# Kernel tuning notes

Hardware: AMD Instinct MI355X
Metric: run time of the kernel (lower is better)

Reference implementation:

```python
import jax, jax.numpy as jnp
import numpy as np

N = 50000      # nodes per graph type
E = 600000     # directed edges
F = 64         # raw node feature length
H = 128        # hidden / embedding size (embedding == h, so no padding needed)
STEPS = 4
G = 64         # graphs in batch


def setup_inputs() -> dict:
    key = jax.random.key(0)
    ks = jax.random.split(key, 16)
    s = 1.0 / np.sqrt(H)
    inp = {
        "atom_x": jax.random.normal(ks[0], (N, F), jnp.float32),
        "voro_x": jax.random.normal(ks[1], (N, F), jnp.float32),
        "atom_edge_index": jax.random.randint(ks[2], (2, E), 0, N, jnp.int64),
        "voro_edge_index": jax.random.randint(ks[3], (2, E), 0, N, jnp.int64),
        "batch": jnp.sort(jax.random.randint(ks[4], (N,), 0, G, jnp.int64)),
        # input embeddings (bias=False)
        "W_atom_in": jax.random.normal(ks[5], (F, H), jnp.float32) / np.sqrt(F),
        "W_voro_in": jax.random.normal(ks[6], (F, H), jnp.float32) / np.sqrt(F),
        # GatedGraphConv per-step message weights [STEPS, H, H]
        "atom_W": jax.random.normal(ks[7], (STEPS, H, H), jnp.float32) * s,
        "voro_W": jax.random.normal(ks[8], (STEPS, H, H), jnp.float32) * s,
        # GRUCell params (torch layout: W_ih [3H, H], gates ordered r, z, n)
        "atom_Wih": jax.random.normal(ks[9], (3 * H, H), jnp.float32) * s,
        "atom_Whh": jax.random.normal(ks[10], (3 * H, H), jnp.float32) * s,
        "atom_bih": jnp.zeros((3 * H,), jnp.float32),
        "atom_bhh": jnp.zeros((3 * H,), jnp.float32),
        "voro_Wih": jax.random.normal(ks[11], (3 * H, H), jnp.float32) * s,
        "voro_Whh": jax.random.normal(ks[12], (3 * H, H), jnp.float32) * s,
        "voro_bih": jnp.zeros((3 * H,), jnp.float32),
        "voro_bhh": jnp.zeros((3 * H,), jnp.float32),
        # prediction head Linear(2H, 1)
        "pred_W": jax.random.normal(ks[13], (2 * H, 1), jnp.float32) * s,
        "pred_b": jnp.zeros((1,), jnp.float32),
    }
    return inp


def _gated_graph_conv(x, edge_index, W, Wih, Whh, bih, bhh):
    """PyG GatedGraphConv with aggr='add': per step, m = h @ W_l, scatter-add
    messages from source to target, then GRUCell(m, h)."""
    src, dst = edge_index[0], edge_index[1]

    def step(h, Wl):
        m = h @ Wl                                           # [N, H]
        agg = jax.ops.segment_sum(m[src], dst, num_segments=N)  # gather+scatter-add
        gi = agg @ Wih.T + bih                               # input gates
        gh = h @ Whh.T + bhh                                 # hidden gates
        ir, iz, inn = jnp.split(gi, 3, axis=-1)
        hr, hz, hn = jnp.split(gh, 3, axis=-1)
        r = jax.nn.sigmoid(ir + hr)
        z = jax.nn.sigmoid(iz + hz)
        n = jnp.tanh(inn + r * hn)
        h_new = (1.0 - z) * n + z * h
        return h_new, None

    h, _ = jax.lax.scan(step, x, W)
    return h


def _mean_pool(x, batch):
    s = jax.ops.segment_sum(x, batch, num_segments=G)
    cnt = jax.ops.segment_sum(jnp.ones((x.shape[0],), x.dtype), batch, num_segments=G)
    return s / jnp.maximum(cnt, 1.0)[:, None]


def reference(atom_x, voro_x, atom_edge_index, voro_edge_index, batch,
              W_atom_in, W_voro_in, atom_W, voro_W,
              atom_Wih, atom_Whh, atom_bih, atom_bhh,
              voro_Wih, voro_Whh, voro_bih, voro_bhh,
              pred_W, pred_b):
    a = jnp.tanh(atom_x @ W_atom_in)                         # [N, H]
    v = jnp.tanh(voro_x @ W_voro_in)                         # [N, H]
    a = _gated_graph_conv(a, atom_edge_index, atom_W, atom_Wih, atom_Whh, atom_bih, atom_bhh)
    v = _gated_graph_conv(v, voro_edge_index, voro_W, voro_Wih, voro_Whh, voro_bih, voro_bhh)
    a = jax.nn.relu(_mean_pool(a, batch))                    # [G, H]
    v = jax.nn.relu(_mean_pool(v, batch))                    # [G, H]
    g = jnp.concatenate([a, v], axis=1)                      # [G, 2H]
    return (g @ pred_W + pred_b)[:, 0]                       # [G]
```

## Files before the change

kernel.cpp:

```cpp
#include <hip/hip_runtime.h>
#include <hip/hip_fp16.h>
#include <math.h>

#define HDIM 128
typedef unsigned short u16;
typedef __attribute__((ext_vector_type(8))) short bf16x8;
typedef __attribute__((ext_vector_type(4))) float f32x4;

__device__ __forceinline__ u16 f2bf(float x) {
    unsigned u = __float_as_uint(x);
    u = (u + 0x7FFFu + ((u >> 16) & 1u)) >> 16;
    return (u16)u;
}
__device__ __forceinline__ float bf2f(u16 h) {
    return __uint_as_float(((unsigned)h) << 16);
}
__device__ __forceinline__ bf16x8 ld8(const u16* p) {
    return *reinterpret_cast<const bf16x8*>(p);
}
__device__ __forceinline__ void split8(const float* v, bf16x8& hi, bf16x8& lo) {
#pragma unroll
    for (int j = 0; j < 8; ++j) {
        unsigned u = __float_as_uint(v[j]);
        unsigned h = (u + 0x7FFFu + ((u >> 16) & 1u)) >> 16;
        float rem = v[j] - __uint_as_float(h << 16);
        hi[j] = (short)h;
        lo[j] = (short)(__float_as_uint(rem) >> 16);
    }
}
__device__ __forceinline__ float2 up2(unsigned u) {
    __half2 h = *reinterpret_cast<__half2*>(&u);
    float2 f; f.x = __low2float(h); f.y = __high2float(h); return f;
}
__device__ __forceinline__ u16 f2h(float x) {
    __half t = __float2half(x);
    return *reinterpret_cast<u16*>(&t);
}
#define MFMA(acc, a, b) acc = __builtin_amdgcn_mfma_f32_16x16x32_bf16(a, b, acc, 0, 0, 0)

__global__ __launch_bounds__(256) void prep_wfull(const float* __restrict__ Ws,
                                                  const float* __restrict__ Wih,
                                                  u16* __restrict__ hi, u16* __restrict__ lo) {
    int s = blockIdx.y;
    int idx = blockIdx.x * 256 + threadIdx.x;
    int c2 = idx >> 7, r = idx & 127;
    const float* wr = Ws + (size_t)s * 16384 + (size_t)r * 128;
    const float* wc = Wih + (size_t)c2 * 128;
    float acc = 0.f;
#pragma unroll 8
    for (int k = 0; k < 128; k += 4) {
        float4 a = *reinterpret_cast<const float4*>(wr + k);
        float4 b = *reinterpret_cast<const float4*>(wc + k);
        acc += a.x * b.x + a.y * b.y + a.z * b.z + a.w * b.w;
    }
    size_t o = (size_t)s * 49152 + idx;
    u16 h = f2bf(acc);
    hi[o] = h; lo[o] = f2bf(acc - bf2f(h));
}

__global__ __launch_bounds__(256) void prep_split(const float* __restrict__ W,
                                                  u16* __restrict__ hi, u16* __restrict__ lo, int n) {
    int i = blockIdx.x * 256 + threadIdx.x;
    if (i < n) { float v = W[i]; u16 h = f2bf(v); hi[i] = h; lo[i] = f2bf(v - bf2f(h)); }
}

__global__ __launch_bounds__(256) void prep_win(const float* __restrict__ W,
                                                u16* __restrict__ hi, u16* __restrict__ lo) {
    int idx = blockIdx.x * 256 + threadIdx.x;
    int r = idx >> 6, c = idx & 63;
    float v = W[(size_t)c * 128 + r];
    u16 h = f2bf(v);
    hi[idx] = h; lo[idx] = f2bf(v - bf2f(h));
}

__global__ __launch_bounds__(256) void split_x2(const float* __restrict__ x0, const float* __restrict__ x1,
                                                u16* __restrict__ hi0, u16* __restrict__ lo0,
                                                u16* __restrict__ hi1, u16* __restrict__ lo1,
                                                int n, int ntot) {
    int i = blockIdx.x * 256 + threadIdx.x;
    if (i >= ntot) return;
    const float* x = blockIdx.y ? x1 : x0;
    u16* hi = blockIdx.y ? hi1 : hi0;
    u16* lo = blockIdx.y ? lo1 : lo0;
    float v = (i < n) ? x[i] : 0.f;
    u16 h = f2bf(v);
    hi[i] = h; lo[i] = f2bf(v - bf2f(h));
}

__global__ __launch_bounds__(256) void embed_k(const u16* __restrict__ Xhi0, const u16* __restrict__ Xlo0,
                                               const u16* __restrict__ Xhi1, const u16* __restrict__ Xlo1,
                                               const u16* __restrict__ Bhi0, const u16* __restrict__ Blo0,
                                               const u16* __restrict__ Bhi1, const u16* __restrict__ Blo1,
                                               u16* __restrict__ Hh0, u16* __restrict__ Hh1) {
    const int by = blockIdx.y;
    const u16* Xhi = by ? Xhi1 : Xhi0;  const u16* Xlo = by ? Xlo1 : Xlo0;
    const u16* Bhi = by ? Bhi1 : Bhi0;  const u16* Blo = by ? Blo1 : Blo0;
    u16* Hh = by ? Hh1 : Hh0;
    const int tid = threadIdx.x, wave = tid >> 6, lane = tid & 63;
    const int row0 = blockIdx.x * 32, cs = wave * 32;
    const int lr = lane & 15, lk = (lane >> 4) * 8;
    f32x4 acc[2][2];
#pragma unroll
    for (int i = 0; i < 2; ++i)
#pragma unroll
        for (int j = 0; j < 2; ++j) acc[i][j] = (f32x4)0.f;
#pragma unroll
    for (int kc = 0; kc < 2; ++kc) {
        const size_t ao = (size_t)(row0 + lr) * 64 + kc * 32 + lk;
        bf16x8 ah0 = ld8(Xhi + ao), ah1 = ld8(Xhi + ao + 16 * 64);
        bf16x8 al0 = ld8(Xlo + ao), al1 = ld8(Xlo + ao + 16 * 64);
#pragma unroll
        for (int cf = 0; cf < 2; ++cf) {
            const size_t bo = (size_t)(cs + cf * 16 + lr) * 64 + kc * 32 + lk;
            bf16x8 bh = ld8(Bhi + bo), bl = ld8(Blo + bo);
            MFMA(acc[0][cf], ah0, bh); MFMA(acc[0][cf], ah0, bl); MFMA(acc[0][cf], al0, bh);
            MFMA(acc[1][cf], ah1, bh); MFMA(acc[1][cf], ah1, bl); MFMA(acc[1][cf], al1, bh);
        }
    }
#pragma unroll
    for (int rf = 0; rf < 2; ++rf)
#pragma unroll
        for (int cf = 0; cf < 2; ++cf)
#pragma unroll
            for (int rg = 0; rg < 4; ++rg) {
                int row = row0 + rf * 16 + (lane >> 4) * 4 + rg;
                int col = cs + cf * 16 + lr;
                Hh[(size_t)row * HDIM + col] = f2h(tanhf(acc[rf][cf][rg]));
            }
}

__global__ __launch_bounds__(512, 4) void step_k(const u16* __restrict__ Hh0, const u16* __restrict__ Hh1,
                                                 const int* __restrict__ ro0, const int* __restrict__ ro1,
                                                 const int* __restrict__ ss0, const int* __restrict__ ss1,
                                                 const u16* __restrict__ Wf0h, const u16* __restrict__ Wf0l,
                                                 const u16* __restrict__ Wf1h, const u16* __restrict__ Wf1l,
                                                 const u16* __restrict__ Wh0h, const u16* __restrict__ Wh0l,
                                                 const u16* __restrict__ Wh1h, const u16* __restrict__ Wh1l,
                                                 const float* __restrict__ bi0, const float* __restrict__ bh0,
                                                 const float* __restrict__ bi1, const float* __restrict__ bh1,
                                                 u16* __restrict__ Hn0, u16* __restrict__ Hn1, int Nn) {
    __shared__ u16 agh[32][136];
    __shared__ u16 agl[32][136];
    __shared__ u16 hhh[32][136];
    __shared__ u16 hhl[32][136];
    const int by = blockIdx.y;
    const u16* Hh = by ? Hh1 : Hh0;
    const int* row_off = by ? ro1 : ro0;
    const int* ssrc = by ? ss1 : ss0;
    const int tid = threadIdx.x, wave = tid >> 6, lane = tid & 63;
    const int row0 = blockIdx.x * 32;

#pragma unroll
    for (int q = 0; q < 4; ++q) {
        const int node = row0 + wave * 4 + q;
        float ax = 0.f, ay = 0.f;
        if (node < Nn) {
            const int lo = __builtin_amdgcn_readfirstlane(row_off[node]);
            const int hi = __builtin_amdgcn_readfirstlane(row_off[node + 1]);
            int i = lo;
            for (; i + 8 <= hi; i += 8) {
                unsigned u[8];
#pragma unroll
                for (int j = 0; j < 8; ++j) {
                    const int idx = ssrc[i + j];
                    u[j] = *reinterpret_cast<const unsigned*>(Hh + (size_t)idx * HDIM + lane * 2);
                }
#pragma unroll
                for (int j = 0; j < 8; ++j) { float2 v = up2(u[j]); ax += v.x; ay += v.y; }
            }
            for (; i < hi; ++i) {
                const int idx = ssrc[i];
                float2 v = up2(*reinterpret_cast<const unsigned*>(Hh + (size_t)idx * HDIM + lane * 2));
                ax += v.x; ay += v.y;
            }
        }
        const int nl = wave * 4 + q;
        u16 hx = f2bf(ax), hy = f2bf(ay);
        u16 lx = f2bf(ax - bf2f(hx)), ly = f2bf(ay - bf2f(hy));
        *reinterpret_cast<unsigned*>(&agh[nl][lane * 2]) = (unsigned)hx | ((unsigned)hy << 16);
        *reinterpret_cast<unsigned*>(&agl[nl][lane * 2]) = (unsigned)lx | ((unsigned)ly << 16);
    }

    {
        const int r = tid >> 4, c0 = (tid & 15) * 8;
        float v[8];
        const int row = row0 + r;
        if (row < Nn) {
            const u16* hp = Hh + (size_t)row * HDIM + c0;
#pragma unroll
            for (int j = 0; j < 4; ++j) {
                float2 f = up2(*reinterpret_cast<const unsigned*>(hp + j * 2));
                v[j * 2] = f.x; v[j * 2 + 1] = f.y;
            }
        } else {
#pragma unroll
            for (int j = 0; j < 8; ++j) v[j] = 0.f;
        }
        bf16x8 hi, lo;
        split8(v, hi, lo);
        *reinterpret_cast<bf16x8*>(&hhh[r][c0]) = hi;
        *reinterpret_cast<bf16x8*>(&hhl[r][c0]) = lo;
    }
    __syncthreads();

    const u16* Wfhi = by ? Wf1h : Wf0h;  const u16* Wflo = by ? Wf1l : Wf0l;
    const u16* Whhi = by ? Wh1h : Wh0h;  const u16* Whlo = by ? Wh1l : Wh0l;
    const float* bih = by ? bi1 : bi0;   const float* bhh = by ? bh1 : bh0;
    u16* Hnh = by ? Hn1 : Hn0;
    const int lr = lane & 15, lk = (lane >> 4) * 8, cs = wave * 16;
    f32x4 accI[2][3], accH[2][3];
#pragma unroll
    for (int rf = 0; rf < 2; ++rf)
#pragma unroll
        for (int g = 0; g < 3; ++g) { accI[rf][g] = (f32x4)0.f; accH[rf][g] = (f32x4)0.f; }
#pragma unroll
    for (int kc = 0; kc < 4; ++kc) {
        bf16x8 ga[2], gl[2], ha[2], hl[2];
#pragma unroll
        for (int rf = 0; rf < 2; ++rf) {
            const int rr = rf * 16 + lr, cc = kc * 32 + lk;
            ga[rf] = *reinterpret_cast<const bf16x8*>(&agh[rr][cc]);
            gl[rf] = *reinterpret_cast<const bf16x8*>(&agl[rr][cc]);
            ha[rf] = *reinterpret_cast<const bf16x8*>(&hhh[rr][cc]);
            hl[rf] = *reinterpret_cast<const bf16x8*>(&hhl[rr][cc]);
        }
#pragma unroll
        for (int g = 0; g < 3; ++g) {
            const size_t bo = (size_t)(g * 128 + cs + lr) * HDIM + kc * 32 + lk;
            bf16x8 fh = ld8(Wfhi + bo), fl = ld8(Wflo + bo);
            bf16x8 wh = ld8(Whhi + bo), wl = ld8(Whlo + bo);
#pragma unroll
            for (int rf = 0; rf < 2; ++rf) {
                MFMA(accI[rf][g], ga[rf], fh); MFMA(accI[rf][g], ga[rf], fl); MFMA(accI[rf][g], gl[rf], fh);
                MFMA(accH[rf][g], ha[rf], wh); MFMA(accH[rf][g], ha[rf], wl); MFMA(accH[rf][g], hl[rf], wh);
            }
        }
    }
    const int c = cs + lr;
    const float bir = bih[c], biz = bih[128 + c], bin = bih[256 + c];
    const float bhr = bhh[c], bhz = bhh[128 + c], bhn = bhh[256 + c];
#pragma unroll
    for (int rf = 0; rf < 2; ++rf)
#pragma unroll
        for (int rg = 0; rg < 4; ++rg) {
            const int rl = rf * 16 + (lane >> 4) * 4 + rg;
            const int row = row0 + rl;
            float gir = accI[rf][0][rg] + bir;
            float giz = accI[rf][1][rg] + biz;
            float gin = accI[rf][2][rg] + bin;
            float ghr = accH[rf][0][rg] + bhr;
            float ghz = accH[rf][1][rg] + bhz;
            float ghn = accH[rf][2][rg] + bhn;
            float r = 1.f / (1.f + expf(-(gir + ghr)));
            float z = 1.f / (1.f + expf(-(giz + ghz)));
            float nn = tanhf(gin + r * ghn);
            float hold = bf2f(hhh[rl][c]) + bf2f(hhl[rl][c]);
            float hn = (1.f - z) * nn + z * hold;
            if (row < Nn) Hnh[(size_t)row * HDIM + c] = f2h(hn);
        }
}

__global__ void zero_int2(int* p0, int* p1, int n) {
    int i = blockIdx.x * 256 + threadIdx.x;
    int* p = blockIdx.y ? p1 : p0;
    if (i < n) p[i] = 0;
}

__global__ void hist_k2(const int* __restrict__ d0, const int* __restrict__ d1,
                        int* __restrict__ c0, int* __restrict__ c1, int E) {
    int e = blockIdx.x * 256 + threadIdx.x;
    const int* dst = blockIdx.y ? d1 : d0;
    int* cnt = blockIdx.y ? c1 : c0;
    if (e < E) atomicAdd(&cnt[dst[e]], 1);
}

__global__ __launch_bounds__(1024) void scan_k2(int* __restrict__ c0, int* __restrict__ r0,
                                                int* __restrict__ c1, int* __restrict__ r1, int n) {
    int* cnt_cursor = blockIdx.x ? c1 : c0;
    int* row_off = blockIdx.x ? r1 : r0;
    __shared__ int wsum[16];
    __shared__ int carry_s;
    const int tid = threadIdx.x, lane = tid & 63, wv = tid >> 6;
    if (tid == 0) carry_s = 0;
    __syncthreads();
    for (int base = 0; base < n; base += 1024) {
        int i = base + tid;
        int v = (i < n) ? cnt_cursor[i] : 0;
        int x = v;
#pragma unroll
        for (int off = 1; off < 64; off <<= 1) {
            int t = __shfl_up(x, off);
            if (lane >= off) x += t;
        }
        if (lane == 63) wsum[wv] = x;
        __syncthreads();
        if (wv == 0 && lane < 16) {
            int s = wsum[lane];
#pragma unroll
            for (int off = 1; off < 16; off <<= 1) {
                int t = __shfl_up(s, off);
                if (lane >= off) s += t;
            }
            wsum[lane] = s;
        }
        __syncthreads();
        int wbase = (wv == 0) ? 0 : wsum[wv - 1];
        int carry = carry_s;
        int total = wsum[15];
        int excl = carry + wbase + x - v;
        if (i < n) { row_off[i] = excl; cnt_cursor[i] = excl; }
        __syncthreads();
        if (tid == 0) carry_s = carry + total;
        __syncthreads();
    }
    if (tid == 0) row_off[n] = carry_s;
}

__global__ void scatter_k2(const int* __restrict__ s0, const int* __restrict__ d0,
                           const int* __restrict__ s1, const int* __restrict__ d1,
                           int* __restrict__ c0, int* __restrict__ c1,
                           int* __restrict__ o0, int* __restrict__ o1, int E) {
    int e = blockIdx.x * 256 + threadIdx.x;
    const int* src = blockIdx.y ? s1 : s0;
    const int* dst = blockIdx.y ? d1 : d0;
    int* cursor = blockIdx.y ? c1 : c0;
    int* ssrc = blockIdx.y ? o1 : o0;
    if (e < E) {
        int p = atomicAdd(&cursor[dst[e]], 1);
        ssrc[p] = src[e];
    }
}

__global__ __launch_bounds__(256) void pool_k(const u16* __restrict__ H0, const u16* __restrict__ H1,
                                              const int* __restrict__ batch,
                                              float* __restrict__ p0, float* __restrict__ p1, int M) {
    const u16* Hf = blockIdx.y ? H1 : H0;
    float* pooled = blockIdx.y ? p1 : p0;
    __shared__ int lo_s, hi_s;
    __shared__ float smx[256], smy[256];
    int g = blockIdx.x;
    if (threadIdx.x == 0) {
        int lo = 0, hi = M;
        while (lo < hi) { int mid = (lo + hi) >> 1; if (batch[mid] < g) lo = mid + 1; else hi = mid; }
        lo_s = lo;
        int lo2 = lo, hi2 = M;
        while (lo2 < hi2) { int mid = (lo2 + hi2) >> 1; if (batch[mid] < g + 1) lo2 = mid + 1; else hi2 = mid; }
        hi_s = lo2;
    }
    __syncthreads();
    int lo = lo_s, hi = hi_s;
    int c2 = threadIdx.x & 63, quarter = threadIdx.x >> 6;
    float ax = 0.f, ay = 0.f;
    for (int i = lo + quarter; i < hi; i += 4) {
        float2 v = up2(*reinterpret_cast<const unsigned*>(Hf + (size_t)i * HDIM + c2 * 2));
        ax += v.x; ay += v.y;
    }
    smx[threadIdx.x] = ax; smy[threadIdx.x] = ay;
    __syncthreads();
    if (quarter == 0) {
        float sx = smx[c2] + smx[c2 + 64] + smx[c2 + 128] + smx[c2 + 192];
        float sy = smy[c2] + smy[c2 + 64] + smy[c2 + 128] + smy[c2 + 192];
        float cnt = (float)(hi - lo); if (cnt < 1.f) cnt = 1.f;
        pooled[g * HDIM + c2 * 2]     = fmaxf(sx / cnt, 0.f);
        pooled[g * HDIM + c2 * 2 + 1] = fmaxf(sy / cnt, 0.f);
    }
}

__global__ void pred_kernel(const float* __restrict__ pa, const float* __restrict__ pv,
                            const float* __restrict__ pW, const float* __restrict__ pb,
                            float* __restrict__ out) {
    int g = blockIdx.x, lane = threadIdx.x;
    float s = pa[g * HDIM + lane] * pW[lane]
            + pa[g * HDIM + 64 + lane] * pW[64 + lane]
            + pv[g * HDIM + lane] * pW[HDIM + lane]
            + pv[g * HDIM + 64 + lane] * pW[192 + lane];
    for (int off = 32; off; off >>= 1) s += __shfl_down(s, off);
    if (lane == 0) out[g] = s + pb[0];
}

extern "C" void kernel_launch(void* const* d_in, const int* in_sizes, int n_in,
                              void* d_out, int out_size, void* d_ws, size_t ws_size,
                              hipStream_t stream) {
    const float* atom_x   = (const float*)d_in[0];
    const float* voro_x   = (const float*)d_in[1];
    const int*   atom_ei  = (const int*)d_in[2];
    const int*   voro_ei  = (const int*)d_in[3];
    const int*   batch    = (const int*)d_in[4];
    const float* W_at_in  = (const float*)d_in[5];
    const float* W_vo_in  = (const float*)d_in[6];
    const float* atom_W   = (const float*)d_in[7];
    const float* voro_W   = (const float*)d_in[8];
    const float* atom_Wih = (const float*)d_in[9];
    const float* atom_Whh = (const float*)d_in[10];
    const float* atom_bih = (const float*)d_in[11];
    const float* atom_bhh = (const float*)d_in[12];
    const float* voro_Wih = (const float*)d_in[13];
    const float* voro_Whh = (const float*)d_in[14];
    const float* voro_bih = (const float*)d_in[15];
    const float* voro_bhh = (const float*)d_in[16];
    const float* pred_W   = (const float*)d_in[17];
    const float* pred_b   = (const float*)d_in[18];
    float* out = (float*)d_out;

    const int Nn = in_sizes[4];
    const int Ee = in_sizes[2] / 2;
    const int Gg = out_size;
    const int Npad = (Nn + 31) & ~31;

    char* base = (char*)d_ws;
    size_t off = 0;
    auto alloc = [&](size_t bytes) -> char* {
        char* p = base + off;
        off = (off + bytes + 255) & ~(size_t)255;
        return p;
    };

    u16 *HhA[2], *HhB[2];
    u16 *Xhi[2], *Xlo[2];
    u16 *WfHi[2], *WfLo[2], *WhHi[2], *WhLo[2], *WnHi[2], *WnLo[2];
    int *row_off[2], *cursor[2], *ssrc[2];
    for (int t = 0; t < 2; ++t) {
        HhA[t] = (u16*)alloc((size_t)Npad * HDIM * 2);
        HhB[t] = (u16*)alloc((size_t)Npad * HDIM * 2);
        Xhi[t] = HhB[t];
        Xlo[t] = HhB[t] + (size_t)Npad * 64;
        WfHi[t] = (u16*)alloc(4 * 49152 * 2); WfLo[t] = (u16*)alloc(4 * 49152 * 2);
        WhHi[t] = (u16*)alloc(384 * 128 * 2); WhLo[t] = (u16*)alloc(384 * 128 * 2);
        WnHi[t] = (u16*)alloc(128 * 64 * 2);  WnLo[t] = (u16*)alloc(128 * 64 * 2);
        row_off[t] = (int*)alloc((size_t)(Nn + 1) * 4);
        cursor[t]  = (int*)alloc((size_t)Nn * 4);
        ssrc[t]    = (int*)alloc((size_t)Ee * 4);
    }
    float* pooledA = (float*)alloc((size_t)Gg * HDIM * 4);
    float* pooledV = (float*)alloc((size_t)Gg * HDIM * 4);

    const float* Wst[2] = {atom_W, voro_W};
    const float* Wih[2] = {atom_Wih, voro_Wih};
    const float* Whh[2] = {atom_Whh, voro_Whh};
    const float* Win[2] = {W_at_in, W_vo_in};

    for (int t = 0; t < 2; ++t) {
        prep_wfull<<<dim3(192, 4), 256, 0, stream>>>(Wst[t], Wih[t], WfHi[t], WfLo[t]);
        prep_split<<<192, 256, 0, stream>>>(Whh[t], WhHi[t], WhLo[t], 384 * 128);
        prep_win<<<32, 256, 0, stream>>>(Win[t], WnHi[t], WnLo[t]);
    }

    const int eb  = (Ee + 255) / 256;
    const int nb  = (Nn + 255) / 256;
    const int gbs = Npad / 32;

    split_x2<<<dim3((Npad * 64 + 255) / 256, 2), 256, 0, stream>>>(
        atom_x, voro_x, Xhi[0], Xlo[0], Xhi[1], Xlo[1], Nn * 64, Npad * 64);
    embed_k<<<dim3(gbs, 2), 256, 0, stream>>>(Xhi[0], Xlo[0], Xhi[1], Xlo[1],
                                              WnHi[0], WnLo[0], WnHi[1], WnLo[1],
                                              HhA[0], HhA[1]);

    zero_int2<<<dim3(nb, 2), 256, 0, stream>>>(cursor[0], cursor[1], Nn);
    hist_k2<<<dim3(eb, 2), 256, 0, stream>>>(atom_ei + Ee, voro_ei + Ee, cursor[0], cursor[1], Ee);
    scan_k2<<<2, 1024, 0, stream>>>(cursor[0], row_off[0], cursor[1], row_off[1], Nn);
    scatter_k2<<<dim3(eb, 2), 256, 0, stream>>>(atom_ei, atom_ei + Ee, voro_ei, voro_ei + Ee,
                                                cursor[0], cursor[1], ssrc[0], ssrc[1], Ee);

    u16 *gA0 = HhA[0], *gB0 = HhB[0], *gA1 = HhA[1], *gB1 = HhB[1];
    for (int s = 0; s < 4; ++s) {
        step_k<<<dim3(gbs, 2), 512, 0, stream>>>(
            gA0, gA1, row_off[0], row_off[1], ssrc[0], ssrc[1],
            WfHi[0] + (size_t)s * 49152, WfLo[0] + (size_t)s * 49152,
            WfHi[1] + (size_t)s * 49152, WfLo[1] + (size_t)s * 49152,
            WhHi[0], WhLo[0], WhHi[1], WhLo[1],
            atom_bih, atom_bhh, voro_bih, voro_bhh,
            gB0, gB1, Nn);
        u16* up;
        up = gA0; gA0 = gB0; gB0 = up;
        up = gA1; gA1 = gB1; gB1 = up;
    }
    pool_k<<<dim3(Gg, 2), 256, 0, stream>>>(gA0, gA1, batch, pooledA, pooledV, Nn);
    pred_kernel<<<Gg, 64, 0, stream>>>(pooledA, pooledV, pred_W, pred_b, out);
}
```

Measured before the change: 1.221 ms.

## Stage edge indices in LDS, widen gather loads, fuse input split, parallelize scan

```diff
diff --git a/kernel.cpp b/kernel.cpp
--- a/kernel.cpp
+++ b/kernel.cpp
@@ -35,6 +35,13 @@
 __device__ __forceinline__ u16 f2h(float x) {
     __half t = __float2half(x);
     return *reinterpret_cast<u16*>(&t);
+}
+__device__ __forceinline__ void acc_u4(float* a, uint4 u, float w) {
+    float2 v0 = up2(u.x), v1 = up2(u.y), v2 = up2(u.z), v3 = up2(u.w);
+    a[0] = fmaf(w, v0.x, a[0]); a[1] = fmaf(w, v0.y, a[1]);
+    a[2] = fmaf(w, v1.x, a[2]); a[3] = fmaf(w, v1.y, a[3]);
+    a[4] = fmaf(w, v2.x, a[4]); a[5] = fmaf(w, v2.y, a[5]);
+    a[6] = fmaf(w, v3.x, a[6]); a[7] = fmaf(w, v3.y, a[7]);
 }
 #define MFMA(acc, a, b) acc = __builtin_amdgcn_mfma_f32_16x16x32_bf16(a, b, acc, 0, 0, 0)
 
@@ -73,27 +80,12 @@
     hi[idx] = h; lo[idx] = f2bf(v - bf2f(h));
 }
 
-__global__ __launch_bounds__(256) void split_x2(const float* __restrict__ x0, const float* __restrict__ x1,
-                                                u16* __restrict__ hi0, u16* __restrict__ lo0,
-                                                u16* __restrict__ hi1, u16* __restrict__ lo1,
-                                                int n, int ntot) {
-    int i = blockIdx.x * 256 + threadIdx.x;
-    if (i >= ntot) return;
-    const float* x = blockIdx.y ? x1 : x0;
-    u16* hi = blockIdx.y ? hi1 : hi0;
-    u16* lo = blockIdx.y ? lo1 : lo0;
-    float v = (i < n) ? x[i] : 0.f;
-    u16 h = f2bf(v);
-    hi[i] = h; lo[i] = f2bf(v - bf2f(h));
-}
-
-__global__ __launch_bounds__(256) void embed_k(const u16* __restrict__ Xhi0, const u16* __restrict__ Xlo0,
-                                               const u16* __restrict__ Xhi1, const u16* __restrict__ Xlo1,
+__global__ __launch_bounds__(256) void embed_k(const float* __restrict__ X0, const float* __restrict__ X1,
                                                const u16* __restrict__ Bhi0, const u16* __restrict__ Blo0,
                                                const u16* __restrict__ Bhi1, const u16* __restrict__ Blo1,
-                                               u16* __restrict__ Hh0, u16* __restrict__ Hh1) {
+                                               u16* __restrict__ Hh0, u16* __restrict__ Hh1, int Nn) {
     const int by = blockIdx.y;
-    const u16* Xhi = by ? Xhi1 : Xhi0;  const u16* Xlo = by ? Xlo1 : Xlo0;
+    const float* X = by ? X1 : X0;
     const u16* Bhi = by ? Bhi1 : Bhi0;  const u16* Blo = by ? Blo1 : Blo0;
     u16* Hh = by ? Hh1 : Hh0;
     const int tid = threadIdx.x, wave = tid >> 6, lane = tid & 63;
@@ -106,9 +98,28 @@
         for (int j = 0; j < 2; ++j) acc[i][j] = (f32x4)0.f;
 #pragma unroll
     for (int kc = 0; kc < 2; ++kc) {
-        const size_t ao = (size_t)(row0 + lr) * 64 + kc * 32 + lk;
-        bf16x8 ah0 = ld8(Xhi + ao), ah1 = ld8(Xhi + ao + 16 * 64);
-        bf16x8 al0 = ld8(Xlo + ao), al1 = ld8(Xlo + ao + 16 * 64);
+        float xv[8];
+        bf16x8 ah0, al0, ah1, al1;
+        const int r0i = row0 + lr;
+        if (r0i < Nn) {
+            const float* xp = X + (size_t)r0i * 64 + kc * 32 + lk;
+            *reinterpret_cast<float4*>(&xv[0]) = *reinterpret_cast<const float4*>(xp);
+            *reinterpret_cast<float4*>(&xv[4]) = *reinterpret_cast<const float4*>(xp + 4);
+        } else {
+#pragma unroll
+            for (int j = 0; j < 8; ++j) xv[j] = 0.f;
+        }
+        split8(xv, ah0, al0);
+        const int r1i = row0 + 16 + lr;
+        if (r1i < Nn) {
+            const float* xp = X + (size_t)r1i * 64 + kc * 32 + lk;
+            *reinterpret_cast<float4*>(&xv[0]) = *reinterpret_cast<const float4*>(xp);
+            *reinterpret_cast<float4*>(&xv[4]) = *reinterpret_cast<const float4*>(xp + 4);
+        } else {
+#pragma unroll
+            for (int j = 0; j < 8; ++j) xv[j] = 0.f;
+        }
+        split8(xv, ah1, al1);
 #pragma unroll
         for (int cf = 0; cf < 2; ++cf) {
             const size_t bo = (size_t)(cs + cf * 16 + lr) * 64 + kc * 32 + lk;
@@ -129,7 +140,7 @@
             }
 }
 
-__global__ __launch_bounds__(512, 4) void step_k(const u16* __restrict__ Hh0, const u16* __restrict__ Hh1,
+__global__ __launch_bounds__(512, 8) void step_k(const u16* __restrict__ Hh0, const u16* __restrict__ Hh1,
                                                  const int* __restrict__ ro0, const int* __restrict__ ro1,
                                                  const int* __restrict__ ss0, const int* __restrict__ ss1,
                                                  const u16* __restrict__ Wf0h, const u16* __restrict__ Wf0l,
@@ -143,42 +154,65 @@
     __shared__ u16 agl[32][136];
     __shared__ u16 hhh[32][136];
     __shared__ u16 hhl[32][136];
+    __shared__ int eidx[1024];
     const int by = blockIdx.y;
     const u16* Hh = by ? Hh1 : Hh0;
     const int* row_off = by ? ro1 : ro0;
     const int* ssrc = by ? ss1 : ss0;
     const int tid = threadIdx.x, wave = tid >> 6, lane = tid & 63;
     const int row0 = blockIdx.x * 32;
+    const int g16 = lane >> 4, l16 = lane & 15;
+
+    const int rowEnd = (row0 + 32 < Nn) ? row0 + 32 : Nn;
+    const int eLo = row_off[row0];
+    const int nE = row_off[rowEnd] - eLo;
+    for (int i = tid; i < nE && i < 1024; i += 512) eidx[i] = ssrc[eLo + i];
+    __syncthreads();
 
 #pragma unroll
     for (int q = 0; q < 4; ++q) {
-        const int node = row0 + wave * 4 + q;
-        float ax = 0.f, ay = 0.f;
+        const int nl = wave * 4 + q;
+        const int node = row0 + nl;
+        float a8[8];
+#pragma unroll
+        for (int j = 0; j < 8; ++j) a8[j] = 0.f;
         if (node < Nn) {
-            const int lo = __builtin_amdgcn_readfirstlane(row_off[node]);
-            const int hi = __builtin_amdgcn_readfirstlane(row_off[node + 1]);
-            int i = lo;
-            for (; i + 8 <= hi; i += 8) {
-                unsigned u[8];
-#pragma unroll
-                for (int j = 0; j < 8; ++j) {
-                    const int idx = ssrc[i + j];
-                    u[j] = *reinterpret_cast<const unsigned*>(Hh + (size_t)idx * HDIM + lane * 2);
+            const int lo = row_off[node] - eLo;
+            const int hi = row_off[node + 1] - eLo;
+            if (hi > lo) {
+                uint4 u[4]; float w[4];
+#pragma unroll
+                for (int b = 0; b < 4; ++b) {
+                    const int p = lo + b * 4 + g16;
+                    const bool val = p < hi;
+                    const int ps = val ? p : lo;
+                    const int idx = (ps < 1024) ? eidx[ps] : ssrc[eLo + ps];
+                    u[b] = *reinterpret_cast<const uint4*>(Hh + (size_t)idx * HDIM + l16 * 8);
+                    w[b] = val ? 1.f : 0.f;
                 }
 #pragma unroll
-                for (int j = 0; j < 8; ++j) { float2 v = up2(u[j]); ax += v.x; ay += v.y; }
+                for (int b = 0; b < 4; ++b) acc_u4(a8, u[b], w[b]);
+                for (int i = lo + 16; i < hi; i += 4) {
+                    const int p = i + g16;
+                    const bool val = p < hi;
+                    const int ps = val ? p : lo;
+                    const int idx = (ps < 1024) ? eidx[ps] : ssrc[eLo + ps];
+                    uint4 uu = *reinterpret_cast<const uint4*>(Hh + (size_t)idx * HDIM + l16 * 8);
+                    acc_u4(a8, uu, val ? 1.f : 0.f);
+                }
             }
-            for (; i < hi; ++i) {
-                const int idx = ssrc[i];
-                float2 v = up2(*reinterpret_cast<const unsigned*>(Hh + (size_t)idx * HDIM + lane * 2));
-                ax += v.x; ay += v.y;
-            }
-        }
-        const int nl = wave * 4 + q;
-        u16 hx = f2bf(ax), hy = f2bf(ay);
-        u16 lx = f2bf(ax - bf2f(hx)), ly = f2bf(ay - bf2f(hy));
-        *reinterpret_cast<unsigned*>(&agh[nl][lane * 2]) = (unsigned)hx | ((unsigned)hy << 16);
-        *reinterpret_cast<unsigned*>(&agl[nl][lane * 2]) = (unsigned)lx | ((unsigned)ly << 16);
+        }
+#pragma unroll
+        for (int j = 0; j < 8; ++j) {
+            a8[j] += __shfl_xor(a8[j], 16);
+            a8[j] += __shfl_xor(a8[j], 32);
+        }
+        if (g16 == 0) {
+            bf16x8 h8, l8;
+            split8(a8, h8, l8);
+            *reinterpret_cast<bf16x8*>(&agh[nl][l16 * 8]) = h8;
+            *reinterpret_cast<bf16x8*>(&agl[nl][l16 * 8]) = l8;
+        }
     }
 
     {
@@ -274,46 +308,58 @@
     if (e < E) atomicAdd(&cnt[dst[e]], 1);
 }
 
-__global__ __launch_bounds__(1024) void scan_k2(int* __restrict__ c0, int* __restrict__ r0,
-                                                int* __restrict__ c1, int* __restrict__ r1, int n) {
-    int* cnt_cursor = blockIdx.x ? c1 : c0;
-    int* row_off = blockIdx.x ? r1 : r0;
-    __shared__ int wsum[16];
-    __shared__ int carry_s;
+__global__ __launch_bounds__(256) void scan_part(const int* __restrict__ c0, const int* __restrict__ c1,
+                                                 int* __restrict__ r0, int* __restrict__ r1,
+                                                 int* __restrict__ bt0, int* __restrict__ bt1, int n) {
+    const int* cnt = blockIdx.y ? c1 : c0;
+    int* ro = blockIdx.y ? r1 : r0;
+    int* bt = blockIdx.y ? bt1 : bt0;
+    __shared__ int wsum[4];
     const int tid = threadIdx.x, lane = tid & 63, wv = tid >> 6;
-    if (tid == 0) carry_s = 0;
+    const int i0 = blockIdx.x * 1024 + tid * 4;
+    int v[4];
+#pragma unroll
+    for (int j = 0; j < 4; ++j) v[j] = (i0 + j < n) ? cnt[i0 + j] : 0;
+    int s = v[0] + v[1] + v[2] + v[3];
+    int x = s;
+#pragma unroll
+    for (int off = 1; off < 64; off <<= 1) { int t = __shfl_up(x, off); if (lane >= off) x += t; }
+    if (lane == 63) wsum[wv] = x;
     __syncthreads();
-    for (int base = 0; base < n; base += 1024) {
-        int i = base + tid;
-        int v = (i < n) ? cnt_cursor[i] : 0;
-        int x = v;
-#pragma unroll
-        for (int off = 1; off < 64; off <<= 1) {
-            int t = __shfl_up(x, off);
-            if (lane >= off) x += t;
-        }
-        if (lane == 63) wsum[wv] = x;
-        __syncthreads();
-        if (wv == 0 && lane < 16) {
-            int s = wsum[lane];
-#pragma unroll
-            for (int off = 1; off < 16; off <<= 1) {
-                int t = __shfl_up(s, off);
-                if (lane >= off) s += t;
-            }
-            wsum[lane] = s;
-        }
-        __syncthreads();
-        int wbase = (wv == 0) ? 0 : wsum[wv - 1];
-        int carry = carry_s;
-        int total = wsum[15];
-        int excl = carry + wbase + x - v;
-        if (i < n) { row_off[i] = excl; cnt_cursor[i] = excl; }
-        __syncthreads();
-        if (tid == 0) carry_s = carry + total;
-        __syncthreads();
-    }
-    if (tid == 0) row_off[n] = carry_s;
+    int wbase = 0;
+#pragma unroll
+    for (int w = 0; w < 4; ++w) wbase += (w < wv) ? wsum[w] : 0;
+    int run = wbase + x - s;
+#pragma unroll
+    for (int j = 0; j < 4; ++j) { if (i0 + j < n) ro[i0 + j] = run; run += v[j]; }
+    if (tid == 255) bt[blockIdx.x] = wbase + x;
+}
+
+__global__ void scan_tops(int* __restrict__ bt0, int* __restrict__ bt1, int nb) {
+    int* bt = blockIdx.x ? bt1 : bt0;
+    const int lane = threadIdx.x;
+    int v = (lane < nb) ? bt[lane] : 0;
+    int x = v;
+#pragma unroll
+    for (int off = 1; off < 64; off <<= 1) { int t = __shfl_up(x, off); if (lane >= off) x += t; }
+    if (lane < nb) bt[lane] = x - v;
+    if (lane == 63) bt[nb] = x;
+}
+
+__global__ void scan_fix(int* __restrict__ r0, int* __restrict__ r1,
+                         const int* __restrict__ bt0, const int* __restrict__ bt1,
+                         int* __restrict__ cur0, int* __restrict__ cur1, int n, int nb) {
+    const int i = blockIdx.x * 256 + threadIdx.x;
+    int* ro = blockIdx.y ? r1 : r0;
+    const int* bt = blockIdx.y ? bt1 : bt0;
+    int* cur = blockIdx.y ? cur1 : cur0;
+    if (i < n) {
+        int val = ro[i] + bt[i >> 10];
+        ro[i] = val;
+        cur[i] = val;
+    } else if (i == n) {
+        ro[n] = bt[nb];
+    }
 }
 
 __global__ void scatter_k2(const int* __restrict__ s0, const int* __restrict__ d0,
@@ -406,6 +452,7 @@
     const int Ee = in_sizes[2] / 2;
     const int Gg = out_size;
     const int Npad = (Nn + 31) & ~31;
+    const int nbScan = (Nn + 1023) / 1024;
 
     char* base = (char*)d_ws;
     size_t off = 0;
@@ -416,20 +463,18 @@
     };
 
     u16 *HhA[2], *HhB[2];
-    u16 *Xhi[2], *Xlo[2];
     u16 *WfHi[2], *WfLo[2], *WhHi[2], *WhLo[2], *WnHi[2], *WnLo[2];
-    int *row_off[2], *cursor[2], *ssrc[2];
+    int *row_off[2], *cursor[2], *ssrc[2], *bt[2];
     for (int t = 0; t < 2; ++t) {
         HhA[t] = (u16*)alloc((size_t)Npad * HDIM * 2);
         HhB[t] = (u16*)alloc((size_t)Npad * HDIM * 2);
-        Xhi[t] = HhB[t];
-        Xlo[t] = HhB[t] + (size_t)Npad * 64;
         WfHi[t] = (u16*)alloc(4 * 49152 * 2); WfLo[t] = (u16*)alloc(4 * 49152 * 2);
         WhHi[t] = (u16*)alloc(384 * 128 * 2); WhLo[t] = (u16*)alloc(384 * 128 * 2);
         WnHi[t] = (u16*)alloc(128 * 64 * 2);  WnLo[t] = (u16*)alloc(128 * 64 * 2);
         row_off[t] = (int*)alloc((size_t)(Nn + 1) * 4);
         cursor[t]  = (int*)alloc((size_t)Nn * 4);
         ssrc[t]    = (int*)alloc((size_t)Ee * 4);
+        bt[t]      = (int*)alloc((size_t)(nbScan + 1) * 4);
     }
     float* pooledA = (float*)alloc((size_t)Gg * HDIM * 4);
     float* pooledV = (float*)alloc((size_t)Gg * HDIM * 4);
@@ -449,15 +494,17 @@
     const int nb  = (Nn + 255) / 256;
     const int gbs = Npad / 32;
 
-    split_x2<<<dim3((Npad * 64 + 255) / 256, 2), 256, 0, stream>>>(
-        atom_x, voro_x, Xhi[0], Xlo[0], Xhi[1], Xlo[1], Nn * 64, Npad * 64);
-    embed_k<<<dim3(gbs, 2), 256, 0, stream>>>(Xhi[0], Xlo[0], Xhi[1], Xlo[1],
+    embed_k<<<dim3(gbs, 2), 256, 0, stream>>>(atom_x, voro_x,
                                               WnHi[0], WnLo[0], WnHi[1], WnLo[1],
-                                              HhA[0], HhA[1]);
+                                              HhA[0], HhA[1], Nn);
 
     zero_int2<<<dim3(nb, 2), 256, 0, stream>>>(cursor[0], cursor[1], Nn);
     hist_k2<<<dim3(eb, 2), 256, 0, stream>>>(atom_ei + Ee, voro_ei + Ee, cursor[0], cursor[1], Ee);
-    scan_k2<<<2, 1024, 0, stream>>>(cursor[0], row_off[0], cursor[1], row_off[1], Nn);
+    scan_part<<<dim3(nbScan, 2), 256, 0, stream>>>(cursor[0], cursor[1], row_off[0], row_off[1],
+                                                   bt[0], bt[1], Nn);
+    scan_tops<<<2, 64, 0, stream>>>(bt[0], bt[1], nbScan);
+    scan_fix<<<dim3((Nn + 1 + 255) / 256, 2), 256, 0, stream>>>(row_off[0], row_off[1], bt[0], bt[1],
+                                                                cursor[0], cursor[1], Nn, nbScan);
     scatter_k2<<<dim3(eb, 2), 256, 0, stream>>>(atom_ei, atom_ei + Ee, voro_ei, voro_ei + Ee,
                                                 cursor[0], cursor[1], ssrc[0], ssrc[1], Ee);
 
```

New measurement: 1.603 ms. +31.2%, slower.
